# Optimization experiments

Measured on AMD Instinct MI355X. Metric: run time of the kernel, lower is better.

The kernel has to match this reference:

```python
import jax, jax.numpy as jnp
import numpy as np

STRIDES = (8.0, 16.0, 32.0)
ANCHORS = np.array([[[12,16],[19,36],[40,28]],
                    [[36,75],[76,55],[72,146]],
                    [[142,110],[192,243],[459,401]]], dtype=np.float32)  # [3 levels, 3 anchors, 2] in input pixels
INPUT_SIZE = 416.0
IGNORE_THRESHOLD = 0.5
EPS = 1e-7
MAX_BOXES = 64  # fixed cap on true boxes per image for jit-able ignore-mask
NC = 80


def _bce_logits(logits, targets):
    # numerically-stable binary cross entropy with logits, elementwise
    return jnp.maximum(logits, 0.0) - logits * targets + jnp.log1p(jnp.exp(-jnp.abs(logits)))


def _iou_xywh(b1, b2):
    # center-format boxes, broadcastable; returns IoU over last dim pair
    a1 = b1[..., 2] * b1[..., 3]
    a2 = b2[..., 2] * b2[..., 3]
    lt = jnp.maximum(b1[..., :2] - b1[..., 2:] * 0.5, b2[..., :2] - b2[..., 2:] * 0.5)
    rb = jnp.minimum(b1[..., :2] + b1[..., 2:] * 0.5, b2[..., :2] + b2[..., 2:] * 0.5)
    wh = jnp.maximum(rb - lt, 0.0)
    inter = wh[..., 0] * wh[..., 1]
    union = a1 + a2 - inter
    return inter / jnp.maximum(union, 1e-9)


def _level_loss(feature, label, idx):
    N, C, H, W = feature.shape
    f = feature.transpose(0, 2, 3, 1).reshape(N, H, W, 3, -1)
    raw_xy, raw_wh = f[..., 0:2], f[..., 2:4]
    raw_conf, raw_prob = f[..., 4:5], f[..., 5:]

    label_xywh = label[..., 0:4]
    label_conf = label[..., 4:5]
    label_prob = label[..., 5:]

    stride = STRIDES[idx]
    anchors = jnp.asarray(ANCHORS[idx])  # [3,2]

    gy, gx = jnp.meshgrid(jnp.arange(H, dtype=f.dtype), jnp.arange(W, dtype=f.dtype), indexing='ij')
    grid = jnp.stack([gx, gy], axis=-1)[:, :, None, :]  # [H,W,1,2]

    # decode predictions (GeneratePrediction)
    pred_xy = (jax.nn.sigmoid(raw_xy) + grid) * stride
    pred_wh = jnp.exp(raw_wh) * anchors
    pred_xywh = jnp.concatenate([pred_xy, pred_wh], axis=-1)  # [N,H,W,3,4]

    xy_offset = label_xywh[..., :2] / stride - grid
    wh_offset = label_conf * jnp.log(label_xywh[..., 2:4] / anchors + EPS)
    bbox_loss_scale = 2.0 - label_xywh[..., 2:3] * label_xywh[..., 3:4] / (INPUT_SIZE * INPUT_SIZE)

    # ignore mask: max IoU of each prediction against this image's true boxes
    conf_flat = label_conf[..., 0].reshape(N, -1)          # [N, H*W*3]
    boxes_flat = label_xywh.reshape(N, -1, 4)              # [N, H*W*3, 4]
    k = min(MAX_BOXES, conf_flat.shape[1])
    vals, idxs = jax.lax.top_k(conf_flat, k)               # positives first (conf is 0/1)
    true_boxes = jnp.take_along_axis(boxes_flat, idxs[..., None], axis=1)  # [N,k,4]
    valid = vals > 0.0                                     # [N,k]
    iou = _iou_xywh(pred_xywh[..., None, :], true_boxes[:, None, None, None, :, :])  # [N,H,W,3,k]
    iou = jnp.where(valid[:, None, None, None, :], iou, 0.0)
    max_iou = jnp.max(iou, axis=-1)                        # [N,H,W,3]; 0 when no valid boxes
    ignore_mask = (max_iou < IGNORE_THRESHOLD).astype(f.dtype)[..., None]

    xy_loss = label_conf * bbox_loss_scale * _bce_logits(raw_xy, xy_offset)
    wh_loss = label_conf * bbox_loss_scale * 0.5 * jnp.square(raw_wh - wh_offset)
    bce_conf = _bce_logits(raw_conf, label_conf)
    conf_loss = label_conf * bce_conf + (1.0 - label_conf) * ignore_mask * bce_conf
    prob_loss = label_conf * _bce_logits(raw_prob, label_prob)

    sum_axes = (1, 2, 3, 4)
    reg = jnp.mean(jnp.sum(xy_loss, axis=sum_axes)) + jnp.mean(jnp.sum(wh_loss, axis=sum_axes))
    conf = jnp.mean(jnp.sum(conf_loss, axis=sum_axes))
    prob = jnp.mean(jnp.sum(prob_loss, axis=sum_axes))
    return reg, conf, prob


def _make_label(key, N, H, W, p_pos):
    kc, kxy, kwh, kp = jax.random.split(key, 4)
    conf = (jax.random.uniform(kc, (N, H, W, 3, 1)) < p_pos).astype(jnp.float32)
    xy = jax.random.uniform(kxy, (N, H, W, 3, 2)) * INPUT_SIZE
    wh = jax.random.uniform(kwh, (N, H, W, 3, 2)) * 190.0 + 10.0  # strictly positive
    prob = (jax.random.uniform(kp, (N, H, W, 3, NC)) < 0.0125).astype(jnp.float32)
    return jnp.concatenate([xy, wh, conf, prob], axis=-1)


def setup_inputs() -> dict:
    key = jax.random.key(0)
    ks = jax.random.split(key, 6)
    N, C = 16, 3 * (5 + NC)
    sizes = [52, 26, 13]
    preds = [jax.random.normal(ks[i], (N, C, s, s), dtype=jnp.float32) for i, s in enumerate(sizes)]
    labels = [_make_label(ks[3 + i], N, s, s, 0.0008) for i, s in enumerate(sizes)]
    return {"pred0": preds[0], "pred1": preds[1], "pred2": preds[2],
            "label0": labels[0], "label1": labels[1], "label2": labels[2]}


def reference(pred0, pred1, pred2, label0, label1, label2):
    reg = conf = prob = 0.0
    for i, (f, l) in enumerate([(pred0, label0), (pred1, label1), (pred2, label2)]):
        r, c, p = _level_loss(f, l, i)
        reg, conf, prob = reg + r, conf + c, prob + p
    return (reg, conf, prob)
```

## Files before the change

### kernel.cpp

```cpp
#include <hip/hip_runtime.h>


#define NIMG 16
#define MAXB 64

#define C0 (16 * 3 * 52 * 52)
#define C1 (16 * 3 * 26 * 26)
#define C2 (16 * 3 * 13 * 13)
#define CTOT (C0 + C1 + C2)
#define NBLK ((CTOT + 255) / 256)

#define T0 (C0 * 85 / 4)
#define T1 (C1 * 85 / 4)
#define T2 (C2 * 85 / 4)
#define TTOT (T0 + T1 + T2)

#define SCAN_BLOCKS 1024
#define SCAN_BATCH 4
#define SCAN_NT (SCAN_BLOCKS * 256)

#define WS_COUNTS   0
#define WS_BOXES    256
#define WS_CELLIDS  49408
#define WS_PARTIAL  65536

__device__ __constant__ float d_anchors[3][3][2] = {
    {{12.f, 16.f}, {19.f, 36.f}, {40.f, 28.f}},
    {{36.f, 75.f}, {76.f, 55.f}, {72.f, 146.f}},
    {{142.f, 110.f}, {192.f, 243.f}, {459.f, 401.f}}};

__device__ __forceinline__ float bce_logits(float x, float t) {
    return fmaxf(x, 0.f) - x * t + log1pf(expf(-fabsf(x)));
}

__global__ void scan_labels(const float* __restrict__ l0,
                            const float* __restrict__ l1,
                            const float* __restrict__ l2,
                            int* __restrict__ counts,
                            float4* __restrict__ boxes,
                            int* __restrict__ cellids) {
    int tid = blockIdx.x * blockDim.x + threadIdx.x;
    for (int base = tid; base < TTOT; base += SCAN_BATCH * SCAN_NT) {
        float4 v[SCAN_BATCH];
        #pragma unroll
        for (int k = 0; k < SCAN_BATCH; ++k) {
            int gi = base + k * SCAN_NT;
            if (gi < TTOT) {
                const float* p; int i;
                if (gi < T0)           { p = l0; i = gi; }
                else if (gi < T0 + T1) { p = l1; i = gi - T0; }
                else                   { p = l2; i = gi - T0 - T1; }
                v[k] = ((const float4*)p)[i];
            }
        }
        #pragma unroll
        for (int k = 0; k < SCAN_BATCH; ++k) {
            int gi = base + k * SCAN_NT;
            if (gi >= TTOT) continue;
            unsigned r = (4u * (unsigned)gi) % 85u;
            if (r < 1u || r > 4u) continue;
            int j = 4 - (int)r;
            float c = (j == 0) ? v[k].x : (j == 1) ? v[k].y : (j == 2) ? v[k].z : v[k].w;
            if (c <= 0.f) continue;
            unsigned recg = (4u * (unsigned)gi + (unsigned)j) / 85u;
            int level, cell, hw3; const float* lab;
            if ((int)recg < C0)           { level = 0; cell = (int)recg;           lab = l0; hw3 = 3 * 52 * 52; }
            else if ((int)recg < C0 + C1) { level = 1; cell = (int)recg - C0;      lab = l1; hw3 = 3 * 26 * 26; }
            else                          { level = 2; cell = (int)recg - C0 - C1; lab = l2; hw3 = 3 * 13 * 13; }
            int n = cell / hw3;
            int p = atomicAdd(&counts[level * NIMG + n], 1);
            if (p < MAXB) {
                const float* lp = lab + (size_t)cell * 85;
                float4 b;
                b.x = lp[0]; b.y = lp[1]; b.z = lp[2]; b.w = lp[3];
                boxes[(level * NIMG + n) * MAXB + p] = b;
                cellids[(level * NIMG + n) * MAXB + p] = cell;
            }
        }
    }
}

__global__ void conf_loss(const float* __restrict__ f0,
                          const float* __restrict__ f1,
                          const float* __restrict__ f2,
                          const int* __restrict__ counts,
                          const float4* __restrict__ boxes,
                          const int* __restrict__ cellids,
                          float* __restrict__ partial) {
    int gid = blockIdx.x * blockDim.x + threadIdx.x;
    float conf = 0.f;

    if (gid < CTOT) {
        const float* f;
        int level, cell, W, HW;
        float stride;
        if (gid < C0)           { level = 0; cell = gid;           f = f0; W = 52; HW = 52 * 52; stride = 8.f; }
        else if (gid < C0 + C1) { level = 1; cell = gid - C0;      f = f1; W = 26; HW = 26 * 26; stride = 16.f; }
        else                    { level = 2; cell = gid - C0 - C1; f = f2; W = 13; HW = 13 * 13; stride = 32.f; }

        int hw = cell % HW;
        int na = cell / HW;
        int a = na % 3;
        int n = na / 3;
        int w = hw % W;
        int h = hw / W;
        int cell_lab = (n * HW + hw) * 3 + a;

        const float* fp = f + (size_t)n * 255 * HW + (size_t)a * 85 * HW + hw;
        float rx = fp[0];
        float ry = fp[HW];
        float rw = fp[2 * HW];
        float rh = fp[3 * HW];
        float rc = fp[4 * HW];

        float aw = d_anchors[level][a][0];
        float ah = d_anchors[level][a][1];
        float px = (1.f / (1.f + expf(-rx)) + (float)w) * stride;
        float py = (1.f / (1.f + expf(-ry)) + (float)h) * stride;
        float pw = expf(rw) * aw;
        float ph = expf(rh) * ah;

        int m = counts[level * NIMG + n];
        if (m > MAXB) m = MAXB;
        int base = (level * NIMG + n) * MAXB;
        float parea = pw * ph;
        float pl = px - pw * 0.5f, pr = px + pw * 0.5f;
        float pt = py - ph * 0.5f, pb = py + ph * 0.5f;
        float maxiou = 0.f;
        bool ispos = false;
        for (int i = 0; i < m; ++i) {
            float4 b = boxes[base + i];
            if (cellids[base + i] == cell_lab) ispos = true;
            float tl = b.x - b.z * 0.5f, tr = b.x + b.z * 0.5f;
            float tt = b.y - b.w * 0.5f, tb = b.y + b.w * 0.5f;
            float iw = fmaxf(fminf(pr, tr) - fmaxf(pl, tl), 0.f);
            float ih = fmaxf(fminf(pb, tb) - fmaxf(pt, tt), 0.f);
            float inter = iw * ih;
            float uni = parea + b.z * b.w - inter;
            float iou = inter / fmaxf(uni, 1e-9f);
            maxiou = fmaxf(maxiou, iou);
        }
        if (ispos)              conf = bce_logits(rc, 1.f);
        else if (maxiou < 0.5f) conf = bce_logits(rc, 0.f);
    }

    for (int off = 32; off > 0; off >>= 1) conf += __shfl_down(conf, off);
    __shared__ float s[4];
    int lane = threadIdx.x & 63;
    int wid = threadIdx.x >> 6;
    if (lane == 0) s[wid] = conf;
    __syncthreads();
    if (threadIdx.x == 0)
        partial[1 * 1024 + blockIdx.x] = s[0] + s[1] + s[2] + s[3];
}

__global__ void pos_loss(const float* __restrict__ f0,
                         const float* __restrict__ f1,
                         const float* __restrict__ f2,
                         const float* __restrict__ l0,
                         const float* __restrict__ l1,
                         const float* __restrict__ l2,
                         const int* __restrict__ counts,
                         const float4* __restrict__ boxes,
                         const int* __restrict__ cellids,
                         float* __restrict__ partial) {
    int level = blockIdx.x / NIMG;
    int n = blockIdx.x % NIMG;
    const float *f, *lab;
    int W, HW; float stride;
    if (level == 0)      { f = f0; lab = l0; W = 52; HW = 52 * 52; stride = 8.f; }
    else if (level == 1) { f = f1; lab = l1; W = 26; HW = 26 * 26; stride = 16.f; }
    else                 { f = f2; lab = l2; W = 13; HW = 13 * 13; stride = 32.f; }

    int m = counts[blockIdx.x];
    if (m > MAXB) m = MAXB;
    int bbase = blockIdx.x * MAXB;

    int lane = threadIdx.x & 63;
    int wid = threadIdx.x >> 6;
    float reg_acc = 0.f, prob_acc = 0.f;

    for (int i = wid; i < m; i += 4) {
        int cell = cellids[bbase + i];
        float4 b = boxes[bbase + i];
        int a = cell % 3;
        int hw = (cell / 3) % HW;
        int w = hw % W;
        int h = hw / W;
        const float* fp = f + ((size_t)n * 255 + (size_t)a * 85) * HW + hw;
        const float* lp = lab + (size_t)cell * 85;

        int ch1 = (lane < 40) ? (5 + lane) : ((lane < 44) ? (lane - 40) : 0);
        float g1 = fp[(size_t)ch1 * HW];
        float g2 = fp[(size_t)((lane < 40) ? (45 + lane) : 0) * HW];
        float t1 = lp[(lane < 40) ? (5 + lane) : 0];
        float t2 = lp[(lane < 40) ? (45 + lane) : 0];

        float pp = (lane < 40) ? (bce_logits(g1, t1) + bce_logits(g2, t2)) : 0.f;
        for (int off = 32; off > 0; off >>= 1) pp += __shfl_down(pp, off);

        float rx = __shfl(g1, 40);
        float ry = __shfl(g1, 41);
        float rw = __shfl(g1, 42);
        float rh = __shfl(g1, 43);
        if (lane == 0) {
            prob_acc += pp;
            float aw = d_anchors[level][a][0];
            float ah = d_anchors[level][a][1];
            float ox = b.x / stride - (float)w;
            float oy = b.y / stride - (float)h;
            float ow = logf(b.z / aw + 1e-7f);
            float oh = logf(b.w / ah + 1e-7f);
            float scale = 2.f - b.z * b.w * (1.f / (416.f * 416.f));
            float dw = rw - ow, dh = rh - oh;
            reg_acc += scale * (bce_logits(rx, ox) + bce_logits(ry, oy))
                     + scale * 0.5f * (dw * dw + dh * dh);
        }
    }

    __shared__ float s[2][4];
    if (lane == 0) { s[0][wid] = reg_acc; s[1][wid] = prob_acc; }
    __syncthreads();
    if (threadIdx.x == 0) {
        partial[0 * 1024 + blockIdx.x] = s[0][0] + s[0][1] + s[0][2] + s[0][3];
        partial[2 * 1024 + blockIdx.x] = s[1][0] + s[1][1] + s[1][2] + s[1][3];
    }
}

__global__ void finalize(const float* __restrict__ partial,
                         float* __restrict__ out) {
    float a0 = 0.f, a1 = 0.f, a2 = 0.f;
    for (int i = threadIdx.x; i < NBLK; i += 256) {
        a1 += partial[1 * 1024 + i];
        if (i < 48) {
            a0 += partial[0 * 1024 + i];
            a2 += partial[2 * 1024 + i];
        }
    }
    for (int off = 32; off > 0; off >>= 1) {
        a0 += __shfl_down(a0, off);
        a1 += __shfl_down(a1, off);
        a2 += __shfl_down(a2, off);
    }
    __shared__ float s[3][4];
    int lane = threadIdx.x & 63;
    int wid = threadIdx.x >> 6;
    if (lane == 0) { s[0][wid] = a0; s[1][wid] = a1; s[2][wid] = a2; }
    __syncthreads();
    if (threadIdx.x == 0) {
        out[0] = (s[0][0] + s[0][1] + s[0][2] + s[0][3]) * (1.f / 16.f);
        out[1] = (s[1][0] + s[1][1] + s[1][2] + s[1][3]) * (1.f / 16.f);
        out[2] = (s[2][0] + s[2][1] + s[2][2] + s[2][3]) * (1.f / 16.f);
    }
}

extern "C" void kernel_launch(void* const* d_in, const int* in_sizes, int n_in,
                              void* d_out, int out_size, void* d_ws, size_t ws_size,
                              hipStream_t stream) {
    const float* f0 = (const float*)d_in[0];
    const float* f1 = (const float*)d_in[1];
    const float* f2 = (const float*)d_in[2];
    const float* l0 = (const float*)d_in[3];
    const float* l1 = (const float*)d_in[4];
    const float* l2 = (const float*)d_in[5];
    float* out = (float*)d_out;

    int*    counts  = (int*)((char*)d_ws + WS_COUNTS);
    float4* boxes   = (float4*)((char*)d_ws + WS_BOXES);
    int*    cellids = (int*)((char*)d_ws + WS_CELLIDS);
    float*  partial = (float*)((char*)d_ws + WS_PARTIAL);

    hipMemsetAsync(d_ws, 0, 256, stream);

    scan_labels<<<SCAN_BLOCKS, 256, 0, stream>>>(l0, l1, l2, counts, boxes, cellids);
    conf_loss<<<NBLK, 256, 0, stream>>>(f0, f1, f2, counts, boxes, cellids, partial);
    pos_loss<<<48, 256, 0, stream>>>(f0, f1, f2, l0, l1, l2,
                                     counts, boxes, cellids, partial);
    finalize<<<1, 256, 0, stream>>>(partial, out);
}
```

Measured before the change: 143.5 us.

## Scan labels by confidence field only and fuse conf and positive loss kernels

The label scan no longer streams every float4 of the full label tensors. It now launches one thread per anchor record, which reads only the confidence value at offset 4 and the box when positive, cutting that pass from full-bandwidth reading to strided sparse reads. The conf-loss and positive-loss kernels are merged into one launch, with the extra blocks handling per-image positives, which removes a kernel launch and lets the small positive pass overlap the conf pass. The risk is that strided 4-byte reads at an 85-float stride still touch most cache lines, so the scan may read about as many sectors as before while using less coalesced access.

```diff
diff --git a/kernel.cpp b/kernel.cpp
--- a/kernel.cpp
+++ b/kernel.cpp
@@ -9,15 +9,6 @@
 #define C2 (16 * 3 * 13 * 13)
 #define CTOT (C0 + C1 + C2)
 #define NBLK ((CTOT + 255) / 256)
-
-#define T0 (C0 * 85 / 4)
-#define T1 (C1 * 85 / 4)
-#define T2 (C2 * 85 / 4)
-#define TTOT (T0 + T1 + T2)
-
-#define SCAN_BLOCKS 1024
-#define SCAN_BATCH 4
-#define SCAN_NT (SCAN_BLOCKS * 256)
 
 #define WS_COUNTS   0
 #define WS_BOXES    256
@@ -39,191 +30,167 @@
                             int* __restrict__ counts,
                             float4* __restrict__ boxes,
                             int* __restrict__ cellids) {
-    int tid = blockIdx.x * blockDim.x + threadIdx.x;
-    for (int base = tid; base < TTOT; base += SCAN_BATCH * SCAN_NT) {
-        float4 v[SCAN_BATCH];
-        #pragma unroll
-        for (int k = 0; k < SCAN_BATCH; ++k) {
-            int gi = base + k * SCAN_NT;
-            if (gi < TTOT) {
-                const float* p; int i;
-                if (gi < T0)           { p = l0; i = gi; }
-                else if (gi < T0 + T1) { p = l1; i = gi - T0; }
-                else                   { p = l2; i = gi - T0 - T1; }
-                v[k] = ((const float4*)p)[i];
-            }
-        }
-        #pragma unroll
-        for (int k = 0; k < SCAN_BATCH; ++k) {
-            int gi = base + k * SCAN_NT;
-            if (gi >= TTOT) continue;
-            unsigned r = (4u * (unsigned)gi) % 85u;
-            if (r < 1u || r > 4u) continue;
-            int j = 4 - (int)r;
-            float c = (j == 0) ? v[k].x : (j == 1) ? v[k].y : (j == 2) ? v[k].z : v[k].w;
-            if (c <= 0.f) continue;
-            unsigned recg = (4u * (unsigned)gi + (unsigned)j) / 85u;
-            int level, cell, hw3; const float* lab;
-            if ((int)recg < C0)           { level = 0; cell = (int)recg;           lab = l0; hw3 = 3 * 52 * 52; }
-            else if ((int)recg < C0 + C1) { level = 1; cell = (int)recg - C0;      lab = l1; hw3 = 3 * 26 * 26; }
-            else                          { level = 2; cell = (int)recg - C0 - C1; lab = l2; hw3 = 3 * 13 * 13; }
-            int n = cell / hw3;
-            int p = atomicAdd(&counts[level * NIMG + n], 1);
-            if (p < MAXB) {
-                const float* lp = lab + (size_t)cell * 85;
-                float4 b;
-                b.x = lp[0]; b.y = lp[1]; b.z = lp[2]; b.w = lp[3];
-                boxes[(level * NIMG + n) * MAXB + p] = b;
-                cellids[(level * NIMG + n) * MAXB + p] = cell;
-            }
-        }
-    }
-}
-
-__global__ void conf_loss(const float* __restrict__ f0,
-                          const float* __restrict__ f1,
-                          const float* __restrict__ f2,
-                          const int* __restrict__ counts,
-                          const float4* __restrict__ boxes,
-                          const int* __restrict__ cellids,
-                          float* __restrict__ partial) {
-    int gid = blockIdx.x * blockDim.x + threadIdx.x;
-    float conf = 0.f;
-
-    if (gid < CTOT) {
-        const float* f;
-        int level, cell, W, HW;
-        float stride;
-        if (gid < C0)           { level = 0; cell = gid;           f = f0; W = 52; HW = 52 * 52; stride = 8.f; }
-        else if (gid < C0 + C1) { level = 1; cell = gid - C0;      f = f1; W = 26; HW = 26 * 26; stride = 16.f; }
-        else                    { level = 2; cell = gid - C0 - C1; f = f2; W = 13; HW = 13 * 13; stride = 32.f; }
-
-        int hw = cell % HW;
-        int na = cell / HW;
-        int a = na % 3;
-        int n = na / 3;
-        int w = hw % W;
-        int h = hw / W;
-        int cell_lab = (n * HW + hw) * 3 + a;
-
-        const float* fp = f + (size_t)n * 255 * HW + (size_t)a * 85 * HW + hw;
-        float rx = fp[0];
-        float ry = fp[HW];
-        float rw = fp[2 * HW];
-        float rh = fp[3 * HW];
-        float rc = fp[4 * HW];
-
-        float aw = d_anchors[level][a][0];
-        float ah = d_anchors[level][a][1];
-        float px = (1.f / (1.f + expf(-rx)) + (float)w) * stride;
-        float py = (1.f / (1.f + expf(-ry)) + (float)h) * stride;
-        float pw = expf(rw) * aw;
-        float ph = expf(rh) * ah;
-
-        int m = counts[level * NIMG + n];
-        if (m > MAXB) m = MAXB;
-        int base = (level * NIMG + n) * MAXB;
-        float parea = pw * ph;
-        float pl = px - pw * 0.5f, pr = px + pw * 0.5f;
-        float pt = py - ph * 0.5f, pb = py + ph * 0.5f;
-        float maxiou = 0.f;
-        bool ispos = false;
-        for (int i = 0; i < m; ++i) {
-            float4 b = boxes[base + i];
-            if (cellids[base + i] == cell_lab) ispos = true;
-            float tl = b.x - b.z * 0.5f, tr = b.x + b.z * 0.5f;
-            float tt = b.y - b.w * 0.5f, tb = b.y + b.w * 0.5f;
-            float iw = fmaxf(fminf(pr, tr) - fmaxf(pl, tl), 0.f);
-            float ih = fmaxf(fminf(pb, tb) - fmaxf(pt, tt), 0.f);
-            float inter = iw * ih;
-            float uni = parea + b.z * b.w - inter;
-            float iou = inter / fmaxf(uni, 1e-9f);
-            maxiou = fmaxf(maxiou, iou);
-        }
-        if (ispos)              conf = bce_logits(rc, 1.f);
-        else if (maxiou < 0.5f) conf = bce_logits(rc, 0.f);
-    }
-
-    for (int off = 32; off > 0; off >>= 1) conf += __shfl_down(conf, off);
-    __shared__ float s[4];
+    int rec = blockIdx.x * blockDim.x + threadIdx.x;
+    if (rec >= CTOT) return;
+
+    const float* lab;
+    int level, cell, hw3;
+    if (rec < C0)           { level = 0; cell = rec;           lab = l0; hw3 = 3 * 52 * 52; }
+    else if (rec < C0 + C1) { level = 1; cell = rec - C0;      lab = l1; hw3 = 3 * 26 * 26; }
+    else                    { level = 2; cell = rec - C0 - C1; lab = l2; hw3 = 3 * 13 * 13; }
+
+    const float* lp = lab + (size_t)cell * 85;
+    float c = lp[4];
+    if (c > 0.f) {
+        int n = cell / hw3;
+        int p = atomicAdd(&counts[level * NIMG + n], 1);
+        if (p < MAXB) {
+            float4 b;
+            b.x = lp[0]; b.y = lp[1]; b.z = lp[2]; b.w = lp[3];
+            boxes[(level * NIMG + n) * MAXB + p] = b;
+            cellids[(level * NIMG + n) * MAXB + p] = cell;
+        }
+    }
+}
+
+__global__ void loss_fused(const float* __restrict__ f0,
+                           const float* __restrict__ f1,
+                           const float* __restrict__ f2,
+                           const float* __restrict__ l0,
+                           const float* __restrict__ l1,
+                           const float* __restrict__ l2,
+                           const int* __restrict__ counts,
+                           const float4* __restrict__ boxes,
+                           const int* __restrict__ cellids,
+                           float* __restrict__ partial) {
     int lane = threadIdx.x & 63;
     int wid = threadIdx.x >> 6;
-    if (lane == 0) s[wid] = conf;
-    __syncthreads();
-    if (threadIdx.x == 0)
-        partial[1 * 1024 + blockIdx.x] = s[0] + s[1] + s[2] + s[3];
-}
-
-__global__ void pos_loss(const float* __restrict__ f0,
-                         const float* __restrict__ f1,
-                         const float* __restrict__ f2,
-                         const float* __restrict__ l0,
-                         const float* __restrict__ l1,
-                         const float* __restrict__ l2,
-                         const int* __restrict__ counts,
-                         const float4* __restrict__ boxes,
-                         const int* __restrict__ cellids,
-                         float* __restrict__ partial) {
-    int level = blockIdx.x / NIMG;
-    int n = blockIdx.x % NIMG;
-    const float *f, *lab;
-    int W, HW; float stride;
-    if (level == 0)      { f = f0; lab = l0; W = 52; HW = 52 * 52; stride = 8.f; }
-    else if (level == 1) { f = f1; lab = l1; W = 26; HW = 26 * 26; stride = 16.f; }
-    else                 { f = f2; lab = l2; W = 13; HW = 13 * 13; stride = 32.f; }
-
-    int m = counts[blockIdx.x];
-    if (m > MAXB) m = MAXB;
-    int bbase = blockIdx.x * MAXB;
-
-    int lane = threadIdx.x & 63;
-    int wid = threadIdx.x >> 6;
-    float reg_acc = 0.f, prob_acc = 0.f;
-
-    for (int i = wid; i < m; i += 4) {
-        int cell = cellids[bbase + i];
-        float4 b = boxes[bbase + i];
-        int a = cell % 3;
-        int hw = (cell / 3) % HW;
-        int w = hw % W;
-        int h = hw / W;
-        const float* fp = f + ((size_t)n * 255 + (size_t)a * 85) * HW + hw;
-        const float* lp = lab + (size_t)cell * 85;
-
-        int ch1 = (lane < 40) ? (5 + lane) : ((lane < 44) ? (lane - 40) : 0);
-        float g1 = fp[(size_t)ch1 * HW];
-        float g2 = fp[(size_t)((lane < 40) ? (45 + lane) : 0) * HW];
-        float t1 = lp[(lane < 40) ? (5 + lane) : 0];
-        float t2 = lp[(lane < 40) ? (45 + lane) : 0];
-
-        float pp = (lane < 40) ? (bce_logits(g1, t1) + bce_logits(g2, t2)) : 0.f;
-        for (int off = 32; off > 0; off >>= 1) pp += __shfl_down(pp, off);
-
-        float rx = __shfl(g1, 40);
-        float ry = __shfl(g1, 41);
-        float rw = __shfl(g1, 42);
-        float rh = __shfl(g1, 43);
-        if (lane == 0) {
-            prob_acc += pp;
+
+    if (blockIdx.x < NBLK) {
+        int gid = blockIdx.x * blockDim.x + threadIdx.x;
+        float conf = 0.f;
+
+        if (gid < CTOT) {
+            const float* f;
+            int level, cell, W, HW;
+            float stride;
+            if (gid < C0)           { level = 0; cell = gid;           f = f0; W = 52; HW = 52 * 52; stride = 8.f; }
+            else if (gid < C0 + C1) { level = 1; cell = gid - C0;      f = f1; W = 26; HW = 26 * 26; stride = 16.f; }
+            else                    { level = 2; cell = gid - C0 - C1; f = f2; W = 13; HW = 13 * 13; stride = 32.f; }
+
+            int hw = cell % HW;
+            int na = cell / HW;
+            int a = na % 3;
+            int n = na / 3;
+            int w = hw % W;
+            int h = hw / W;
+            int cell_lab = (n * HW + hw) * 3 + a;
+
+            const float* fp = f + (size_t)n * 255 * HW + (size_t)a * 85 * HW + hw;
+            float rx = fp[0];
+            float ry = fp[HW];
+            float rw = fp[2 * HW];
+            float rh = fp[3 * HW];
+            float rc = fp[4 * HW];
+
             float aw = d_anchors[level][a][0];
             float ah = d_anchors[level][a][1];
-            float ox = b.x / stride - (float)w;
-            float oy = b.y / stride - (float)h;
-            float ow = logf(b.z / aw + 1e-7f);
-            float oh = logf(b.w / ah + 1e-7f);
-            float scale = 2.f - b.z * b.w * (1.f / (416.f * 416.f));
-            float dw = rw - ow, dh = rh - oh;
-            reg_acc += scale * (bce_logits(rx, ox) + bce_logits(ry, oy))
-                     + scale * 0.5f * (dw * dw + dh * dh);
-        }
-    }
-
-    __shared__ float s[2][4];
-    if (lane == 0) { s[0][wid] = reg_acc; s[1][wid] = prob_acc; }
-    __syncthreads();
-    if (threadIdx.x == 0) {
-        partial[0 * 1024 + blockIdx.x] = s[0][0] + s[0][1] + s[0][2] + s[0][3];
-        partial[2 * 1024 + blockIdx.x] = s[1][0] + s[1][1] + s[1][2] + s[1][3];
+            float px = (1.f / (1.f + expf(-rx)) + (float)w) * stride;
+            float py = (1.f / (1.f + expf(-ry)) + (float)h) * stride;
+            float pw = expf(rw) * aw;
+            float ph = expf(rh) * ah;
+
+            int m = counts[level * NIMG + n];
+            if (m > MAXB) m = MAXB;
+            int base = (level * NIMG + n) * MAXB;
+            float parea = pw * ph;
+            float pl = px - pw * 0.5f, pr = px + pw * 0.5f;
+            float pt = py - ph * 0.5f, pb = py + ph * 0.5f;
+            float maxiou = 0.f;
+            bool ispos = false;
+            for (int i = 0; i < m; ++i) {
+                float4 b = boxes[base + i];
+                if (cellids[base + i] == cell_lab) ispos = true;
+                float tl = b.x - b.z * 0.5f, tr = b.x + b.z * 0.5f;
+                float tt = b.y - b.w * 0.5f, tb = b.y + b.w * 0.5f;
+                float iw = fmaxf(fminf(pr, tr) - fmaxf(pl, tl), 0.f);
+                float ih = fmaxf(fminf(pb, tb) - fmaxf(pt, tt), 0.f);
+                float inter = iw * ih;
+                float uni = parea + b.z * b.w - inter;
+                float iou = inter / fmaxf(uni, 1e-9f);
+                maxiou = fmaxf(maxiou, iou);
+            }
+            if (ispos)              conf = bce_logits(rc, 1.f);
+            else if (maxiou < 0.5f) conf = bce_logits(rc, 0.f);
+        }
+
+        for (int off = 32; off > 0; off >>= 1) conf += __shfl_down(conf, off);
+        __shared__ float sc[4];
+        if (lane == 0) sc[wid] = conf;
+        __syncthreads();
+        if (threadIdx.x == 0)
+            partial[1 * 1024 + blockIdx.x] = sc[0] + sc[1] + sc[2] + sc[3];
+
+    } else {
+        int pb = blockIdx.x - NBLK;
+        int level = pb / NIMG;
+        int n = pb % NIMG;
+        const float *f, *lab;
+        int W, HW; float stride;
+        if (level == 0)      { f = f0; lab = l0; W = 52; HW = 52 * 52; stride = 8.f; }
+        else if (level == 1) { f = f1; lab = l1; W = 26; HW = 26 * 26; stride = 16.f; }
+        else                 { f = f2; lab = l2; W = 13; HW = 13 * 13; stride = 32.f; }
+
+        int m = counts[pb];
+        if (m > MAXB) m = MAXB;
+        int bbase = pb * MAXB;
+
+        float reg_acc = 0.f, prob_acc = 0.f;
+        for (int i = wid; i < m; i += 4) {
+            int cell = cellids[bbase + i];
+            float4 b = boxes[bbase + i];
+            int a = cell % 3;
+            int hw = (cell / 3) % HW;
+            int w = hw % W;
+            int h = hw / W;
+            const float* fp = f + ((size_t)n * 255 + (size_t)a * 85) * HW + hw;
+            const float* lp = lab + (size_t)cell * 85;
+
+            int ch1 = (lane < 40) ? (5 + lane) : ((lane < 44) ? (lane - 40) : 0);
+            float g1 = fp[(size_t)ch1 * HW];
+            float g2 = fp[(size_t)((lane < 40) ? (45 + lane) : 0) * HW];
+            float t1 = lp[(lane < 40) ? (5 + lane) : 0];
+            float t2 = lp[(lane < 40) ? (45 + lane) : 0];
+
+            float pp = (lane < 40) ? (bce_logits(g1, t1) + bce_logits(g2, t2)) : 0.f;
+            for (int off = 32; off > 0; off >>= 1) pp += __shfl_down(pp, off);
+
+            float rx = __shfl(g1, 40);
+            float ry = __shfl(g1, 41);
+            float rw = __shfl(g1, 42);
+            float rh = __shfl(g1, 43);
+            if (lane == 0) {
+                prob_acc += pp;
+                float aw = d_anchors[level][a][0];
+                float ah = d_anchors[level][a][1];
+                float ox = b.x / stride - (float)w;
+                float oy = b.y / stride - (float)h;
+                float ow = logf(b.z / aw + 1e-7f);
+                float oh = logf(b.w / ah + 1e-7f);
+                float scale = 2.f - b.z * b.w * (1.f / (416.f * 416.f));
+                float dw = rw - ow, dh = rh - oh;
+                reg_acc += scale * (bce_logits(rx, ox) + bce_logits(ry, oy))
+                         + scale * 0.5f * (dw * dw + dh * dh);
+            }
+        }
+
+        __shared__ float sp[2][4];
+        if (lane == 0) { sp[0][wid] = reg_acc; sp[1][wid] = prob_acc; }
+        __syncthreads();
+        if (threadIdx.x == 0) {
+            partial[0 * 1024 + pb] = sp[0][0] + sp[0][1] + sp[0][2] + sp[0][3];
+            partial[2 * 1024 + pb] = sp[1][0] + sp[1][1] + sp[1][2] + sp[1][3];
+        }
     }
 }
 
@@ -272,9 +239,8 @@
 
     hipMemsetAsync(d_ws, 0, 256, stream);
 
-    scan_labels<<<SCAN_BLOCKS, 256, 0, stream>>>(l0, l1, l2, counts, boxes, cellids);
-    conf_loss<<<NBLK, 256, 0, stream>>>(f0, f1, f2, counts, boxes, cellids, partial);
-    pos_loss<<<48, 256, 0, stream>>>(f0, f1, f2, l0, l1, l2,
-                                     counts, boxes, cellids, partial);
+    scan_labels<<<NBLK, 256, 0, stream>>>(l0, l1, l2, counts, boxes, cellids);
+    loss_fused<<<NBLK + 48, 256, 0, stream>>>(f0, f1, f2, l0, l1, l2,
+                                              counts, boxes, cellids, partial);
     finalize<<<1, 256, 0, stream>>>(partial, out);
 }
```

Result: faster. 134.3 us (-6.5%).
